# Optimization experiments

Hardware: AMD Instinct MI355X
Metric: run time of the kernel (lower is better)

## Reference

```python
import jax, jax.numpy as jnp
import numpy as np

B, NQ, ISIZE = 8, 2048, 1024
H, D, NA = 8, 128, 8            # num_head, attn_dim, num_anchor
AH = H * D                      # ahsize = 1024
ASZ = NA * D                    # anchor_size = 1024
FH = 4096                       # _fhsize
ISZ_NET = FH * H // NA          # 4096, input dim of self.net
EPS = 1e-6


def setup_inputs() -> dict:
    key = jax.random.key(0)
    ks = jax.random.split(key, 12)
    def u(k, shape, fan_in):
        s = 1.0 / np.sqrt(fan_in)
        return jax.random.uniform(k, shape, jnp.float32, -s, s)
    return {
        "inputs": jax.random.normal(ks[0], (B, NQ, ISIZE), jnp.float32),
        "ln_g": jnp.ones((ISIZE,), jnp.float32),
        "ln_b": jnp.zeros((ISIZE,), jnp.float32),
        "q_anchor": u(ks[1], (H, NA, D), D),
        "W_qkv": u(ks[2], (ISIZE, 3 * AH), ISIZE), "b_qkv": jnp.zeros((3 * AH,), jnp.float32),
        "W_an": u(ks[3], (ASZ, FH), ASZ), "b_an": jnp.zeros((FH,), jnp.float32),
        "W_n1": u(ks[4], (ISZ_NET, AH), ISZ_NET), "b_n1": jnp.zeros((AH,), jnp.float32),
        "W_n2": u(ks[5], (AH, FH), AH), "b_n2": jnp.zeros((FH,), jnp.float32),
        "W_n3": u(ks[6], (FH, AH), FH), "b_n3": jnp.zeros((AH,), jnp.float32),
        "W_k": u(ks[7], (AH, AH), AH), "b_k": jnp.zeros((AH,), jnp.float32),
        "W_o": u(ks[8], (AH, ISIZE), AH), "b_o": jnp.zeros((ISIZE,), jnp.float32),
    }


def reference(inputs, ln_g, ln_b, q_anchor, W_qkv, b_qkv, W_an, b_an,
              W_n1, b_n1, W_n2, b_n2, W_n3, b_n3, W_k, b_k, W_o, b_o):
    b, nq = inputs.shape[:2]
    scale = 1.0 / np.sqrt(D)
    # pre-LayerNorm
    mu = jnp.mean(inputs, -1, keepdims=True)
    var = jnp.mean(jnp.square(inputs - mu), -1, keepdims=True)
    x = (inputs - mu) * jax.lax.rsqrt(var + EPS) * ln_g + ln_b
    # QKV projection
    qkv = (x @ W_qkv + b_qkv).reshape(b, nq, 3, H, D)
    q = jnp.transpose(qkv[:, :, 0], (0, 2, 1, 3))   # [b,H,nq,D]
    k = qkv[:, :, 1]                                  # [b,nq,H,D]
    v = qkv[:, :, 2]                                  # [b,nq,H,D]
    # stage 1: fixed anchors attend over the sequence
    sc1 = jax.nn.softmax(jnp.einsum('had,bnhd->bhan', q_anchor, k) * scale, axis=-1)
    out = jnp.einsum('bhan,bnhd->bhad', sc1, v).reshape(b, H, ASZ)   # [b,H,NA*D]
    # anchor_net (share_head Linear + ReLU)
    out = jax.nn.relu(out @ W_an + b_an)                              # [b,H,FH]
    # regroup head-major -> anchor-major
    out = out.reshape(b, H, NA, FH // NA).transpose(0, 2, 1, 3).reshape(b, NA, ISZ_NET)
    # net: bottleneck Linear -> Linear -> ReLU -> Linear
    out = jax.nn.relu((out @ W_n1 + b_n1) @ W_n2 + b_n2) @ W_n3 + b_n3  # [b,NA,AH]
    # stage 2: queries attend over anchors
    kk = (out @ W_k + b_k).reshape(b, NA, H, D)
    sc2 = jax.nn.softmax(jnp.einsum('bhqd,bahd->bhqa', q, kk) * scale, axis=-1)
    ov = out.reshape(b, NA, H, D)
    y = jnp.einsum('bhqa,bahd->bqhd', sc2, ov).reshape(b, nq, AH)
    return y @ W_o + b_o + inputs
```

## Files before the change

### kernel.cpp

```cpp
#include <hip/hip_runtime.h>
#include <cstdint>
#include <cstddef>

typedef unsigned short u16;
typedef __attribute__((ext_vector_type(8))) short short8;
typedef __attribute__((ext_vector_type(4))) float floatx4;
typedef __attribute__((ext_vector_type(16))) float floatx16;

__device__ __forceinline__ u16 f2bf(float f) {
  unsigned u = __float_as_uint(f);
  u += 0x7fffu + ((u >> 16) & 1u);
  return (u16)(u >> 16);
}
__device__ __forceinline__ float bf2f(u16 s) {
  return __uint_as_float(((unsigned)s) << 16);
}

__global__ __launch_bounds__(256) void prep_kernel(const float* __restrict__ x,
                                                   const float* __restrict__ g,
                                                   const float* __restrict__ bta,
                                                   u16* __restrict__ xout,
                                                   const float* __restrict__ Wq,
                                                   u16* __restrict__ WqT,
                                                   const float* __restrict__ Wo,
                                                   u16* __restrict__ WoT,
                                                   const float* __restrict__ b_an,
                                                   const float* __restrict__ b_n1,
                                                   const float* __restrict__ b_n2,
                                                   const float* __restrict__ b_n3,
                                                   const float* __restrict__ b_k,
                                                   float* __restrict__ anp,
                                                   float* __restrict__ h1,
                                                   float* __restrict__ h2,
                                                   float* __restrict__ onet,
                                                   float* __restrict__ kkb) {
  __shared__ float t[32][33];
  __shared__ float red[4], red2[4];
  const int bid = blockIdx.x;
  const int tid = threadIdx.x;
  if (bid < 16384) {
    const int row = bid;
    const float4 v = ((const float4*)(x + (size_t)row * 1024))[tid];
    float s = v.x + v.y + v.z + v.w;
#pragma unroll
    for (int o = 32; o > 0; o >>= 1) s += __shfl_down(s, o);
    const int wv = tid >> 6, ln = tid & 63;
    if (ln == 0) red[wv] = s;
    __syncthreads();
    const float mean = (red[0] + red[1] + red[2] + red[3]) * (1.0f / 1024.0f);
    const float dx = v.x - mean, dy = v.y - mean, dz = v.z - mean, dw = v.w - mean;
    float s2 = dx * dx + dy * dy + dz * dz + dw * dw;
#pragma unroll
    for (int o = 32; o > 0; o >>= 1) s2 += __shfl_down(s2, o);
    if (ln == 0) red2[wv] = s2;
    __syncthreads();
    const float var = (red2[0] + red2[1] + red2[2] + red2[3]) * (1.0f / 1024.0f);
    const float rstd = rsqrtf(var + 1e-6f);
    const float4 gg = ((const float4*)g)[tid];
    const float4 bb = ((const float4*)bta)[tid];
    ushort4 o4;
    o4.x = f2bf(dx * rstd * gg.x + bb.x);
    o4.y = f2bf(dy * rstd * gg.y + bb.y);
    o4.z = f2bf(dz * rstd * gg.z + bb.z);
    o4.w = f2bf(dw * rstd * gg.w + bb.w);
    ((ushort4*)(xout + (size_t)row * 1024))[tid] = o4;
  } else if (bid < 20480) {
    const int t2 = bid - 16384;
    const int xb = t2 & 31, yb0 = t2 >> 5;
    const float* W;
    u16* WT;
    int N, yb;
    if (yb0 < 96) { W = Wq; WT = WqT; N = 3072; yb = yb0; }
    else { W = Wo; WT = WoT; N = 1024; yb = yb0 - 96; }
    const int kb = xb * 32, nb = yb * 32;
    const int tx = tid & 31, ty = tid >> 5;
#pragma unroll
    for (int i = ty; i < 32; i += 8) t[i][tx] = W[(size_t)(kb + i) * N + nb + tx];
    __syncthreads();
#pragma unroll
    for (int i = ty; i < 32; i += 8) WT[(size_t)(nb + i) * 1024 + kb + tx] = f2bf(t[tx][i]);
  } else {
    const int i = (bid - 20480) * 256 + tid;
    if (i < 65536) {
      ((float4*)anp)[i] = ((const float4*)b_an)[i & 1023];
    } else if (i < 81920) {
      const int j = i - 65536;
      ((float4*)h1)[j] = ((const float4*)b_n1)[j & 255];
    } else if (i < 147456) {
      const int j = i - 81920;
      ((float4*)h2)[j] = ((const float4*)b_n2)[j & 1023];
    } else if (i < 163840) {
      const int j = i - 147456;
      ((float4*)onet)[j] = ((const float4*)b_n3)[j & 255];
    } else {
      const int j = i - 163840;
      ((float4*)kkb)[j] = ((const float4*)b_k)[j & 255];
    }
  }
}


__device__ __forceinline__ void stageG(const u16* __restrict__ gp, u16* lp, int K) {
  __builtin_amdgcn_global_load_lds((const __attribute__((address_space(1))) void*)gp,
                                   (__attribute__((address_space(3))) void*)lp, 16, 0, 0);
  __builtin_amdgcn_global_load_lds((const __attribute__((address_space(1))) void*)(gp + ((size_t)K << 6)),
                                   (__attribute__((address_space(3))) void*)(lp + 4096), 16, 0, 0);
}

__device__ __forceinline__ void rdA(short8 (&af)[2][4], const u16* sbuf, const int (&ab)[4],
                                    int halfoff) {
#pragma unroll
  for (int mi = 0; mi < 2; ++mi)
#pragma unroll
    for (int ks = 0; ks < 4; ++ks)
      af[mi][ks] = *(const short8*)(sbuf + halfoff + mi * 2048 + (ab[ks] ^ (mi << 5)));
}
__device__ __forceinline__ void rdB(short8 (&bf)[4], const u16* sbuf, const int (&bb)[4],
                                    int halfoff) {
#pragma unroll
  for (int ks = 0; ks < 4; ++ks)
    bf[ks] = *(const short8*)(sbuf + halfoff + bb[ks]);
}

template <int Q>
__device__ __forceinline__ void mfmaQ(floatx16 (&acc)[4][2], const short8 (&af)[2][4],
                                      const short8 (&bf)[4]) {
#pragma unroll
  for (int ks = 0; ks < 4; ++ks)
#pragma unroll
    for (int mi = 0; mi < 2; ++mi)
      acc[Q][mi] = __builtin_amdgcn_mfma_f32_32x32x16_bf16(af[mi][ks], bf[ks], acc[Q][mi], 0, 0, 0);
}

template <int B_>
__device__ __forceinline__ void gtile(int t, int NT, int K,
                                      u16 (&sA)[2][16384], u16 (&sB)[2][16384],
                                      const u16* gA_lo, const u16* gA_hi,
                                      const u16* gB_lo, const u16* gB_hi,
                                      u16* ldsA_cur, u16* ldsA_alt,
                                      u16* ldsB_cur, u16* ldsB_alt,
                                      const int (&ab)[4], const int (&bb)[4],
                                      floatx16 (&acc)[4][2],
                                      short8 (&afA)[2][4], short8 (&bfP)[4], short8 (&bfN)[4]) {
  rdA(afA, sA[B_], ab, 0);
  __builtin_amdgcn_sched_barrier(0);
  if (t + 1 < NT) stageG(gA_hi + ((t + 1) << 6), ldsA_alt + 8192, K);
  rdB(bfN, sB[B_], bb, 8192);
  asm volatile("s_waitcnt lgkmcnt(4)" ::: "memory");
  __builtin_amdgcn_sched_barrier(0);
  __builtin_amdgcn_s_setprio(1);
  mfmaQ<0>(acc, afA, bfP);
  __builtin_amdgcn_s_setprio(0);
  if (t + 1 < NT) stageG(gB_lo + ((t + 1) << 6), ldsB_alt, K);
  asm volatile("s_waitcnt lgkmcnt(0)" ::: "memory");
  __builtin_amdgcn_sched_barrier(0);
  __builtin_amdgcn_s_setprio(1);
  mfmaQ<1>(acc, afA, bfN);
  __builtin_amdgcn_s_setprio(0);
  rdA(afA, sA[B_], ab, 8192);
  __builtin_amdgcn_s_barrier();
  if (t + 2 < NT) stageG(gA_lo + ((t + 2) << 6), ldsA_cur, K);
  asm volatile("s_waitcnt lgkmcnt(0)" ::: "memory");
  __builtin_amdgcn_sched_barrier(0);
  __builtin_amdgcn_s_setprio(1);
  mfmaQ<2>(acc, afA, bfN);
  __builtin_amdgcn_s_setprio(0);
  if (t + 2 < NT) stageG(gB_hi + ((t + 2) << 6), ldsB_cur + 8192, K);
  if (t + 2 < NT) {
    asm volatile("s_waitcnt vmcnt(4)" ::: "memory");
  } else {
    asm volatile("s_waitcnt vmcnt(0)" ::: "memory");
  }
  __builtin_amdgcn_s_barrier();
  if (t + 1 < NT) rdB(bfN, sB[B_ ^ 1], bb, 0);
  __builtin_amdgcn_sched_barrier(0);
  __builtin_amdgcn_s_setprio(1);
  mfmaQ<3>(acc, afA, bfP);
  __builtin_amdgcn_s_setprio(0);
}

template <int EPI>
__global__ __launch_bounds__(512, 2) void gemm_bf16(const u16* __restrict__ A,
                                                    const u16* __restrict__ BT,
                                                    const float* __restrict__ bias,
                                                    const float* __restrict__ extra,
                                                    u16* __restrict__ outB,
                                                    float* __restrict__ outF,
                                                    int M, int N, int K) {
  __shared__ u16 sA[2][16384];
  __shared__ u16 sB[2][16384];
  const int tid = threadIdx.x;
  const int wave = tid >> 6, lane = tid & 63;
  const int m0 = blockIdx.x * 256, n0 = blockIdx.y * 256;
  const int wr = wave >> 2, wc = wave & 3;
  const int l31 = lane & 31, l5 = lane >> 5, l7 = lane & 7;
  const int NT = K >> 6;

  const int fa = l7 ^ (l31 >> 3);
  const int fb = l7 ^ ((wc * 4 + (l31 >> 3)) & 7);
  int ab[4], bb[4];
#pragma unroll
  for (int ks = 0; ks < 4; ++ks) {
    const int kg = (ks << 1) + l5;
    ab[ks] = (wr * 64 + l31) * 64 + (((kg ^ fa) & 7) << 3);
    bb[ks] = (wc * 32 + l31) * 64 + (((kg ^ fb) & 7) << 3);
  }
  const int srow = wave * 8 + (lane >> 3);
  const int scol = ((lane & 7) ^ (lane >> 3) ^ wave) << 3;
  const u16* gA_lo = A + (size_t)(m0 + srow) * K + scol;
  const u16* gA_hi = A + (size_t)(m0 + 128 + srow) * K + scol;
  const u16* gB_lo = BT + (size_t)(n0 + srow) * K + scol;
  const u16* gB_hi = BT + (size_t)(n0 + 128 + srow) * K + scol;

  floatx16 acc[4][2];
#pragma unroll
  for (int q = 0; q < 4; ++q)
#pragma unroll
    for (int mi = 0; mi < 2; ++mi)
#pragma unroll
      for (int r = 0; r < 16; ++r) acc[q][mi][r] = 0.f;

  stageG(gA_lo, &sA[0][0] + wave * 512, K);
  stageG(gA_hi, &sA[0][8192] + wave * 512, K);
  stageG(gB_lo, &sB[0][0] + wave * 512, K);
  stageG(gB_hi, &sB[0][8192] + wave * 512, K);
  stageG(gA_lo + 64, &sA[1][0] + wave * 512, K);
  stageG(gB_hi + 64, &sB[1][8192] + wave * 512, K);
  asm volatile("s_waitcnt vmcnt(4)" ::: "memory");
  __builtin_amdgcn_s_barrier();

  short8 afA[2][4], bfX[4], bfY[4];
  rdB(bfX, sB[0], bb, 0);
  __builtin_amdgcn_sched_barrier(0);

  for (int t = 0; t < NT; t += 2) {
    gtile<0>(t, NT, K, sA, sB, gA_lo, gA_hi, gB_lo, gB_hi,
             &sA[0][0] + wave * 512, &sA[1][0] + wave * 512,
             &sB[0][0] + wave * 512, &sB[1][0] + wave * 512, ab, bb, acc, afA, bfX, bfY);
    gtile<1>(t + 1, NT, K, sA, sB, gA_lo, gA_hi, gB_lo, gB_hi,
             &sA[1][0] + wave * 512, &sA[0][0] + wave * 512,
             &sB[1][0] + wave * 512, &sB[0][0] + wave * 512, ab, bb, acc, afA, bfY, bfX);
  }

#pragma unroll
  for (int q = 0; q < 4; ++q) {
    const int QM = q >> 1, QN = QM ^ (q & 1);
    const int n = n0 + QN * 128 + wc * 32 + l31;
    const float bs = bias[n];
#pragma unroll
    for (int mi = 0; mi < 2; ++mi) {
      const int mb = m0 + QM * 128 + wr * 64 + mi * 32 + 4 * l5;
#pragma unroll
      for (int reg = 0; reg < 16; ++reg) {
        const int m = mb + (reg & 3) + 8 * (reg >> 2);
        const float v = acc[q][mi][reg] + bs;
        if (EPI == 0)
          outB[(size_t)m * N + n] = f2bf(v);
        else
          outF[(size_t)m * N + n] = v + extra[(size_t)m * N + n];
      }
    }
  }
}

__global__ __launch_bounds__(512) void attn1_fused(const u16* __restrict__ qkv,
                                                   const float* __restrict__ q_anchor,
                                                   float* __restrict__ att1) {
  __shared__ u16 kv[256 * 132];
  __shared__ float S2[2][2048];
  __shared__ float qa2[2][128];
  __shared__ float red[16];
  const int tid = threadIdx.x;
  const int bh = blockIdx.x >> 2, ag = blockIdx.x & 3;
  const int b = bh >> 3, h = bh & 7;
  const int a0 = ag * 2;

  for (int i = tid; i < 256; i += 512)
    qa2[i >> 7][i & 127] = q_anchor[h * 1024 + (a0 + (i >> 7)) * 128 + (i & 127)];

  const float scale = 0.0883883476483184f;
  const size_t rowbase = (size_t)b * 2048;

  {
    const int a = tid >> 8, nn = tid & 255;
    for (int T = 0; T < 8; ++T) {
      __syncthreads();
#pragma unroll
      for (int p = 0; p < 16; ++p) {
        const int c = p * 512 + tid;
        const int r = c >> 5, off = (c & 31) * 4;
        const ushort4 kk = *(const ushort4*)(qkv + (rowbase + T * 256 + r) * 3072 + 1024 + h * 128 + off);
        *(ushort4*)&kv[r * 132 + off] = kk;
      }
      __syncthreads();
      float dot = 0.f;
#pragma unroll 8
      for (int dd = 0; dd < 128; dd += 4) {
        const ushort4 k4 = *(const ushort4*)&kv[nn * 132 + dd];
        const float4 q4 = *(const float4*)&qa2[a][dd];
        dot += q4.x * bf2f(k4.x) + q4.y * bf2f(k4.y) + q4.z * bf2f(k4.z) + q4.w * bf2f(k4.w);
      }
      S2[a][T * 256 + nn] = dot * scale;
    }
  }
  __syncthreads();
  {
    const int a = tid >> 8, li = tid & 255;
    const int wv = (tid >> 6) & 3, ln = tid & 63;
    float mx = -1e30f;
#pragma unroll
    for (int k = 0; k < 8; ++k) mx = fmaxf(mx, S2[a][li + k * 256]);
#pragma unroll
    for (int o = 32; o > 0; o >>= 1) mx = fmaxf(mx, __shfl_xor(mx, o));
    if (ln == 0) red[a * 4 + wv] = mx;
    __syncthreads();
    mx = fmaxf(fmaxf(red[a * 4], red[a * 4 + 1]), fmaxf(red[a * 4 + 2], red[a * 4 + 3]));
    float sum = 0.f;
#pragma unroll
    for (int k = 0; k < 8; ++k) {
      const float e = __expf(S2[a][li + k * 256] - mx);
      S2[a][li + k * 256] = e;
      sum += e;
    }
#pragma unroll
    for (int o = 32; o > 0; o >>= 1) sum += __shfl_xor(sum, o);
    if (ln == 0) red[8 + a * 4 + wv] = sum;
  }
  __syncthreads();
  {
    const int a2 = tid & 1, dq = (tid >> 1) & 31, s = tid >> 6;
    float acc0 = 0.f, acc1 = 0.f, acc2 = 0.f, acc3 = 0.f;
    for (int T = 0; T < 8; ++T) {
      __syncthreads();
#pragma unroll
      for (int p = 0; p < 16; ++p) {
        const int c = p * 512 + tid;
        const int r = c >> 5, off = (c & 31) * 4;
        const ushort4 vv = *(const ushort4*)(qkv + (rowbase + T * 256 + r) * 3072 + 2048 + h * 128 + off);
        *(ushort4*)&kv[r * 132 + off] = vv;
      }
      __syncthreads();
#pragma unroll 4
      for (int j = 0; j < 32; ++j) {
        const int nl = s * 32 + j;
        const float pw = S2[a2][T * 256 + nl];
        const ushort4 v4 = *(const ushort4*)&kv[nl * 132 + dq * 4];
        acc0 += pw * bf2f(v4.x);
        acc1 += pw * bf2f(v4.y);
        acc2 += pw * bf2f(v4.z);
        acc3 += pw * bf2f(v4.w);
      }
    }
    __syncthreads();
    float* scratch = &S2[0][0];
    scratch[((a2 * 32 + dq) * 4 + 0) * 8 + s] = acc0;
    scratch[((a2 * 32 + dq) * 4 + 1) * 8 + s] = acc1;
    scratch[((a2 * 32 + dq) * 4 + 2) * 8 + s] = acc2;
    scratch[((a2 * 32 + dq) * 4 + 3) * 8 + s] = acc3;
  }
  __syncthreads();
  if (tid < 256) {
    const int a2 = tid >> 7, dq = (tid >> 2) & 31, k = tid & 3;
    const float* scratch = &S2[0][0];
    const float* sp = &scratch[((a2 * 32 + dq) * 4 + k) * 8];
    float tot = sp[0] + sp[1] + sp[2] + sp[3] + sp[4] + sp[5] + sp[6] + sp[7];
    const float inv = 1.f / (red[8 + a2 * 4] + red[8 + a2 * 4 + 1] +
                             red[8 + a2 * 4 + 2] + red[8 + a2 * 4 + 3]);
    att1[(size_t)bh * 1024 + (a0 + a2) * 128 + dq * 4 + k] = tot * inv;
  }
}

template <int AMODE>
__global__ __launch_bounds__(256) void mlp_mfma(const float* __restrict__ A,
                                                const float* __restrict__ W,
                                                float* __restrict__ outp,
                                                int K, int N, int KC) {
  __shared__ float sW[64][33];
  const int tid = threadIdx.x;
  const int lane = tid & 63, wave = tid >> 6;
  const int wm = wave * 16;
  const int n0 = blockIdx.x * 64;
  const int kbeg = blockIdx.y * KC;
  const int l15 = lane & 15, kq8 = (lane >> 4) * 8;
  const int arow = wm + l15;

  floatx4 acc[4];
  const floatx4 zero = {0.f, 0.f, 0.f, 0.f};
#pragma unroll
  for (int j = 0; j < 4; ++j) acc[j] = zero;

  for (int kc = 0; kc < KC; kc += 32) {
    const int kbase = kbeg + kc;
    __syncthreads();
#pragma unroll
    for (int p = 0; p < 8; ++p) {
      const int k = p * 4 + wave;
      sW[lane][k] = W[(size_t)(kbase + k) * N + n0 + lane];
    }
    const float* ap;
    if (AMODE == 2) {
      const int k = kbase + kq8;
      ap = A + (size_t)(arow >> 3) * 32768 + (size_t)(k >> 9) * 4096 + (arow & 7) * 512 + (k & 511);
    } else {
      ap = A + (size_t)arow * K + kbase + kq8;
    }
    float4 a0 = *(const float4*)ap;
    float4 a1 = *(const float4*)(ap + 4);
    if (AMODE >= 1) {
      a0.x = fmaxf(a0.x, 0.f); a0.y = fmaxf(a0.y, 0.f);
      a0.z = fmaxf(a0.z, 0.f); a0.w = fmaxf(a0.w, 0.f);
      a1.x = fmaxf(a1.x, 0.f); a1.y = fmaxf(a1.y, 0.f);
      a1.z = fmaxf(a1.z, 0.f); a1.w = fmaxf(a1.w, 0.f);
    }
    short8 af;
    af[0] = (short)f2bf(a0.x); af[1] = (short)f2bf(a0.y);
    af[2] = (short)f2bf(a0.z); af[3] = (short)f2bf(a0.w);
    af[4] = (short)f2bf(a1.x); af[5] = (short)f2bf(a1.y);
    af[6] = (short)f2bf(a1.z); af[7] = (short)f2bf(a1.w);
    __syncthreads();
#pragma unroll
    for (int j = 0; j < 4; ++j) {
      const float* wp = &sW[j * 16 + l15][kq8];
      short8 bf;
      bf[0] = (short)f2bf(wp[0]); bf[1] = (short)f2bf(wp[1]);
      bf[2] = (short)f2bf(wp[2]); bf[3] = (short)f2bf(wp[3]);
      bf[4] = (short)f2bf(wp[4]); bf[5] = (short)f2bf(wp[5]);
      bf[6] = (short)f2bf(wp[6]); bf[7] = (short)f2bf(wp[7]);
      acc[j] = __builtin_amdgcn_mfma_f32_16x16x32_bf16(af, bf, acc[j], 0, 0, 0);
    }
  }
  const int q = lane >> 4;
#pragma unroll
  for (int j = 0; j < 4; ++j)
#pragma unroll
    for (int r = 0; r < 4; ++r) {
      const int m = wm + q * 4 + r;
      const int n = n0 + j * 16 + l15;
      atomicAdd(&outp[(size_t)m * N + n], acc[j][r]);
    }
}

__global__ __launch_bounds__(256) void attn2_kernel(const u16* __restrict__ qkv,
                                                    const float* __restrict__ kk,
                                                    const float* __restrict__ onet,
                                                    u16* __restrict__ y) {
  __shared__ float kkl[8][128];
  __shared__ float ovl[8][128];
  const int tid = threadIdx.x;
  const int chunk = blockIdx.x & 7, bh = blockIdx.x >> 3;
  const int b = bh >> 3, h = bh & 7;
  for (int i = tid; i < 1024; i += 256) {
    const int a = i >> 7, d = i & 127;
    kkl[a][d] = kk[(size_t)(b * 8 + a) * 1024 + h * 128 + d];
    ovl[a][d] = onet[(size_t)(b * 8 + a) * 1024 + h * 128 + d];
  }
  __syncthreads();
  const int n = chunk * 256 + tid;
  const u16* qp = qkv + (size_t)(b * 2048 + n) * 3072 + h * 128;
  float dots[8] = {0, 0, 0, 0, 0, 0, 0, 0};
#pragma unroll 4
  for (int dd = 0; dd < 128; dd += 4) {
    const ushort4 q4 = *(const ushort4*)(qp + dd);
    const float q0 = bf2f(q4.x), q1 = bf2f(q4.y), q2 = bf2f(q4.z), q3 = bf2f(q4.w);
#pragma unroll
    for (int a = 0; a < 8; ++a) {
      const float4 k4 = *(const float4*)&kkl[a][dd];
      dots[a] += k4.x * q0 + k4.y * q1 + k4.z * q2 + k4.w * q3;
    }
  }
  const float scale = 0.0883883476483184f;
  float mx = -1e30f;
#pragma unroll
  for (int a = 0; a < 8; ++a) {
    dots[a] *= scale;
    mx = fmaxf(mx, dots[a]);
  }
  float p[8];
  float sum = 0.f;
#pragma unroll
  for (int a = 0; a < 8; ++a) {
    p[a] = __expf(dots[a] - mx);
    sum += p[a];
  }
  const float inv = 1.f / sum;
#pragma unroll
  for (int a = 0; a < 8; ++a) p[a] *= inv;
  u16* yp = y + (size_t)(b * 2048 + n) * 1024 + h * 128;
#pragma unroll 4
  for (int dd = 0; dd < 128; dd += 4) {
    float a0 = 0, a1 = 0, a2 = 0, a3 = 0;
#pragma unroll
    for (int a = 0; a < 8; ++a) {
      const float4 o4 = *(const float4*)&ovl[a][dd];
      a0 += p[a] * o4.x;
      a1 += p[a] * o4.y;
      a2 += p[a] * o4.z;
      a3 += p[a] * o4.w;
    }
    ushort4 o;
    o.x = f2bf(a0);
    o.y = f2bf(a1);
    o.z = f2bf(a2);
    o.w = f2bf(a3);
    *(ushort4*)(yp + dd) = o;
  }
}

extern "C" void kernel_launch(void* const* d_in, const int* in_sizes, int n_in,
                              void* d_out, int out_size, void* d_ws, size_t ws_size,
                              hipStream_t stream) {
  const float* inputs = (const float*)d_in[0];
  const float* ln_g = (const float*)d_in[1];
  const float* ln_b = (const float*)d_in[2];
  const float* q_anchor = (const float*)d_in[3];
  const float* W_qkv = (const float*)d_in[4];
  const float* b_qkv = (const float*)d_in[5];
  const float* W_an = (const float*)d_in[6];
  const float* b_an = (const float*)d_in[7];
  const float* W_n1 = (const float*)d_in[8];
  const float* b_n1 = (const float*)d_in[9];
  const float* W_n2 = (const float*)d_in[10];
  const float* b_n2 = (const float*)d_in[11];
  const float* W_n3 = (const float*)d_in[12];
  const float* b_n3 = (const float*)d_in[13];
  const float* W_k = (const float*)d_in[14];
  const float* b_k = (const float*)d_in[15];
  const float* W_o = (const float*)d_in[16];
  const float* b_o = (const float*)d_in[17];
  float* out = (float*)d_out;

  char* ws = (char*)d_ws;
  u16* qkv = (u16*)(ws);
  u16* xbf = (u16*)(ws + 100663296);
  u16* WqkvT = (u16*)(ws + 134217728);
  u16* WoT = (u16*)(ws + 140509184);
  float* att1 = (float*)(ws + 142606336);
  float* anp = (float*)(ws + 142868480);
  float* h1 = (float*)(ws + 143917056);
  float* h2 = (float*)(ws + 144179200);
  float* onet = (float*)(ws + 145227776);
  float* kkb = (float*)(ws + 145489920);

  prep_kernel<<<21184, 256, 0, stream>>>(inputs, ln_g, ln_b, xbf,
                                         W_qkv, WqkvT, W_o, WoT,
                                         b_an, b_n1, b_n2, b_n3, b_k,
                                         anp, h1, h2, onet, kkb);
  gemm_bf16<0><<<dim3(64, 12), 512, 0, stream>>>(xbf, WqkvT, b_qkv, nullptr, qkv, nullptr,
                                                 16384, 3072, 1024);
  attn1_fused<<<256, 512, 0, stream>>>(qkv, q_anchor, att1);
  mlp_mfma<0><<<dim3(64, 4), 256, 0, stream>>>(att1, W_an, anp, 1024, 4096, 256);
  mlp_mfma<2><<<dim3(16, 16), 256, 0, stream>>>(anp, W_n1, h1, 4096, 1024, 256);
  mlp_mfma<0><<<dim3(64, 4), 256, 0, stream>>>(h1, W_n2, h2, 1024, 4096, 256);
  mlp_mfma<1><<<dim3(16, 16), 256, 0, stream>>>(h2, W_n3, onet, 4096, 1024, 256);
  mlp_mfma<0><<<dim3(16, 8), 256, 0, stream>>>(onet, W_k, kkb, 1024, 1024, 128);
  attn2_kernel<<<512, 256, 0, stream>>>(qkv, kkb, onet, xbf);
  gemm_bf16<1><<<dim3(64, 4), 512, 0, stream>>>(xbf, WoT, b_o, inputs, nullptr, out,
                                                16384, 1024, 1024);
}
```

Before: 574.7 us.

## Stage attn2 query and output tiles through LDS and split QKV GEMM launch

In attn2, each thread previously read its own 256-byte query row and wrote its own output row with strided per-thread accesses. The block now loads the whole 256-row query tile into padded shared memory with coalesced accesses, reuses that buffer to stage the bf16 outputs, and writes them back coalesced. The QKV GEMM is also split into three launches, each covering one 1024-column slice. This adds about 66KB of LDS per block, which may limit occupancy, and two extra kernel launches.

```diff
diff --git a/kernel.cpp b/kernel.cpp
--- a/kernel.cpp
+++ b/kernel.cpp
@@ -444,6 +444,7 @@
                                                     const float* __restrict__ kk,
                                                     const float* __restrict__ onet,
                                                     u16* __restrict__ y) {
+  __shared__ u16 qv[256 * 132];
   __shared__ float kkl[8][128];
   __shared__ float ovl[8][128];
   const int tid = threadIdx.x;
@@ -454,13 +455,19 @@
     kkl[a][d] = kk[(size_t)(b * 8 + a) * 1024 + h * 128 + d];
     ovl[a][d] = onet[(size_t)(b * 8 + a) * 1024 + h * 128 + d];
   }
+  const int n0 = chunk * 256;
+  const size_t qbase = ((size_t)(b * 2048 + n0)) * 3072 + h * 128;
+#pragma unroll
+  for (int p = 0; p < 32; ++p) {
+    const int c = p * 256 + tid;
+    const int r = c >> 5, off = (c & 31) * 4;
+    *(ushort4*)&qv[r * 132 + off] = *(const ushort4*)(qkv + qbase + (size_t)r * 3072 + off);
+  }
   __syncthreads();
-  const int n = chunk * 256 + tid;
-  const u16* qp = qkv + (size_t)(b * 2048 + n) * 3072 + h * 128;
   float dots[8] = {0, 0, 0, 0, 0, 0, 0, 0};
 #pragma unroll 4
   for (int dd = 0; dd < 128; dd += 4) {
-    const ushort4 q4 = *(const ushort4*)(qp + dd);
+    const ushort4 q4 = *(const ushort4*)&qv[tid * 132 + dd];
     const float q0 = bf2f(q4.x), q1 = bf2f(q4.y), q2 = bf2f(q4.z), q3 = bf2f(q4.w);
 #pragma unroll
     for (int a = 0; a < 8; ++a) {
@@ -475,34 +482,41 @@
     dots[a] *= scale;
     mx = fmaxf(mx, dots[a]);
   }
-  float p[8];
+  float p8[8];
   float sum = 0.f;
 #pragma unroll
   for (int a = 0; a < 8; ++a) {
-    p[a] = __expf(dots[a] - mx);
-    sum += p[a];
+    p8[a] = __expf(dots[a] - mx);
+    sum += p8[a];
   }
   const float inv = 1.f / sum;
 #pragma unroll
-  for (int a = 0; a < 8; ++a) p[a] *= inv;
-  u16* yp = y + (size_t)(b * 2048 + n) * 1024 + h * 128;
+  for (int a = 0; a < 8; ++a) p8[a] *= inv;
 #pragma unroll 4
   for (int dd = 0; dd < 128; dd += 4) {
     float a0 = 0, a1 = 0, a2 = 0, a3 = 0;
 #pragma unroll
     for (int a = 0; a < 8; ++a) {
       const float4 o4 = *(const float4*)&ovl[a][dd];
-      a0 += p[a] * o4.x;
-      a1 += p[a] * o4.y;
-      a2 += p[a] * o4.z;
-      a3 += p[a] * o4.w;
+      a0 += p8[a] * o4.x;
+      a1 += p8[a] * o4.y;
+      a2 += p8[a] * o4.z;
+      a3 += p8[a] * o4.w;
     }
     ushort4 o;
     o.x = f2bf(a0);
     o.y = f2bf(a1);
     o.z = f2bf(a2);
     o.w = f2bf(a3);
-    *(ushort4*)(yp + dd) = o;
+    *(ushort4*)&qv[tid * 132 + dd] = o;
+  }
+  __syncthreads();
+  const size_t ybase = ((size_t)(b * 2048 + n0)) * 1024 + h * 128;
+#pragma unroll
+  for (int p = 0; p < 32; ++p) {
+    const int c = p * 256 + tid;
+    const int r = c >> 5, off = (c & 31) * 4;
+    *(ushort4*)(y + ybase + (size_t)r * 1024 + off) = *(const ushort4*)&qv[r * 132 + off];
   }
 }
 
@@ -545,8 +559,11 @@
                                          W_qkv, WqkvT, W_o, WoT,
                                          b_an, b_n1, b_n2, b_n3, b_k,
                                          anp, h1, h2, onet, kkb);
-  gemm_bf16<0><<<dim3(64, 12), 512, 0, stream>>>(xbf, WqkvT, b_qkv, nullptr, qkv, nullptr,
-                                                 16384, 3072, 1024);
+  for (int c = 0; c < 3; ++c) {
+    gemm_bf16<0><<<dim3(64, 4), 512, 0, stream>>>(
+        xbf, WqkvT + (size_t)c * 1024 * 1024, b_qkv + c * 1024, nullptr,
+        qkv + (size_t)c * 1024, nullptr, 16384, 3072, 1024);
+  }
   attn1_fused<<<256, 512, 0, stream>>>(qkv, q_anchor, att1);
   mlp_mfma<0><<<dim3(64, 4), 256, 0, stream>>>(att1, W_an, anp, 1024, 4096, 256);
   mlp_mfma<2><<<dim3(16, 16), 256, 0, stream>>>(anp, W_n1, h1, 4096, 1024, 256);
```

New measurement: 519.9 us. 1.11x faster.
